# Kernel optimization log

Hardware: AMD Instinct MI355X
Metric: run time of the kernel (lower is better)

The kernel has to match this reference:

```python
import jax, jax.numpy as jnp
import numpy as np

B, T, C = 8, 2048, 1024  # batch, seq_len (== block_size), n_embed
HEAD = 64


def setup_inputs() -> dict:
    key = jax.random.key(0)
    k1, k2, k3, k4 = jax.random.split(key, 4)
    x = jax.random.normal(k1, (B, T, C), dtype=jnp.float32)
    # nn.Linear(n_embed, head_size, bias=False) -> weight [head, C]; stored as [C, head]
    Wk = jax.random.normal(k2, (C, HEAD), dtype=jnp.float32) * (C ** -0.5)
    Wq = jax.random.normal(k3, (C, HEAD), dtype=jnp.float32) * (C ** -0.5)
    Wv = jax.random.normal(k4, (C, HEAD), dtype=jnp.float32) * (C ** -0.5)
    return {"x": x, "Wk": Wk, "Wq": Wq, "Wv": Wv}


def reference(x, Wk, Wq, Wv):
    Bx, Tx, Cx = x.shape
    k = jnp.einsum('btc,ch->bth', x, Wk)  # [B,T,HEAD]
    q = jnp.einsum('btc,ch->bth', x, Wq)
    v = jnp.einsum('btc,ch->bth', x, Wv)
    # Source quirk: scores = k @ q^T (k rows), scaled by n_embed**-0.5 (C, not head_size)
    scores = jnp.einsum('bih,bjh->bij', k, q) * (Cx ** -0.5)  # [B,T,T]
    causal = jnp.tril(jnp.ones((Tx, Tx), dtype=bool))
    scores = jnp.where(causal, scores, -jnp.inf)
    attn = jax.nn.softmax(scores, axis=-1)
    out = jnp.einsum('bij,bjh->bih', attn, v)  # [B,T,HEAD]
    return out
```

## Files before the change

### kernel.cpp

```cpp
#include <hip/hip_runtime.h>
#include <cstdint>

#define B_ 8
#define T_ 2048
#define C_ 1024
#define H_ 64
#define BT_ (B_ * T_)

typedef short short8 __attribute__((ext_vector_type(8)));
typedef short bh4 __attribute__((ext_vector_type(4)));
typedef float f32x4 __attribute__((ext_vector_type(4)));

__device__ inline short f2bf(float f) {
  uint32_t u = __float_as_uint(f);
  u += 0x7fffu + ((u >> 16) & 1u);
  return (short)(u >> 16);
}

__device__ __forceinline__ void gl_lds16(const void* g, void* l) {
  __builtin_amdgcn_global_load_lds(
      (const __attribute__((address_space(1))) unsigned int*)g,
      (__attribute__((address_space(3))) unsigned int*)l, 16, 0, 0);
}

__global__ __launch_bounds__(256) void prep_w(
    const float* __restrict__ Wk, const float* __restrict__ Wq,
    const float* __restrict__ Wv, short* __restrict__ Wt) {
  __shared__ float wl[64][68];
  const int mat = blockIdx.x >> 4;
  const int kc = blockIdx.x & 15;
  const float* W = (mat == 0) ? Wk : (mat == 1) ? Wq : Wv;
  const float sc = (mat == 0) ? 0.03125f * 1.44269504088896f : 1.0f;
  const int t = threadIdx.x;
  const int k0 = kc * 64;
#pragma unroll
  for (int j = 0; j < 4; ++j) {
    int s = t + 256 * j;
    int kr = s >> 4, cf = s & 15;
    float4 v = *reinterpret_cast<const float4*>(&W[(size_t)(k0 + kr) * H_ + cf * 4]);
    wl[kr][cf * 4 + 0] = v.x; wl[kr][cf * 4 + 1] = v.y;
    wl[kr][cf * 4 + 2] = v.z; wl[kr][cf * 4 + 3] = v.w;
  }
  __syncthreads();
#pragma unroll
  for (int j = 0; j < 2; ++j) {
    int s = t + 256 * j;
    int n = s >> 3, g = s & 7;
    short8 o;
#pragma unroll
    for (int i = 0; i < 8; ++i) o[i] = f2bf(wl[8 * g + i][n] * sc);
    *reinterpret_cast<short8*>(&Wt[(size_t)(mat * 64 + n) * C_ + k0 + 8 * g]) = o;
  }
}

__global__ __launch_bounds__(256, 1) void proj_kernel(
    const float* __restrict__ x, const short* __restrict__ Wt,
    short* __restrict__ Kp, short* __restrict__ Qp, short* __restrict__ Vt) {
  __shared__ float xs[2][32 * 64];
  __shared__ short ws[2][192 * 64];
  const int t = threadIdx.x;
  const int w = t >> 6, lane = t & 63;
  const int l15 = lane & 15, lg = lane >> 4;
  const int rg = w >> 1, ch = w & 1;
  const int rowBase = blockIdx.x * 32;

  f32x4 acc[6];
  const f32x4 zf = {0.f, 0.f, 0.f, 0.f};
#pragma unroll
  for (int i = 0; i < 6; ++i) acc[i] = zf;

  auto stage = [&](int buf, int k0) {
#pragma unroll
    for (int j = 0; j < 2; ++j) {
      const int seg = w * 2 + j;
      const int r = seg * 4 + (lane >> 4);
      const float* g =
          &x[(size_t)(rowBase + r) * C_ + k0 + (((lane & 15) ^ (r & 7)) << 2)];
      gl_lds16(g, (char*)&xs[buf][0] + seg * 1024);
    }
#pragma unroll
    for (int j = 0; j < 6; ++j) {
      const int seg = w * 6 + j;
      const int n = seg * 8 + (lane >> 3);
      const short* g =
          &Wt[(size_t)n * C_ + k0 + (((lane & 7) ^ (n & 7)) << 3)];
      gl_lds16(g, (char*)&ws[buf][0] + seg * 1024);
    }
  };

  stage(0, 0);

#pragma unroll 1
  for (int it = 0; it < 16; ++it) {
    __syncthreads();
    const int cb = it & 1;
    if (it < 15) stage(cb ^ 1, (it + 1) * 64);
    const int arow = 16 * rg + l15;
    const int x7 = arow & 7;
    const float* xrow = &xs[cb][arow * 64];
    float4 fa = *reinterpret_cast<const float4*>(xrow + (((2 * lg) ^ x7) << 2));
    float4 fb = *reinterpret_cast<const float4*>(xrow + (((2 * lg + 1) ^ x7) << 2));
    float4 fc = *reinterpret_cast<const float4*>(xrow + (((2 * lg + 8) ^ x7) << 2));
    float4 fd = *reinterpret_cast<const float4*>(xrow + (((2 * lg + 9) ^ x7) << 2));
    short8 a0, a1;
    a0[0] = f2bf(fa.x); a0[1] = f2bf(fa.y); a0[2] = f2bf(fa.z); a0[3] = f2bf(fa.w);
    a0[4] = f2bf(fb.x); a0[5] = f2bf(fb.y); a0[6] = f2bf(fb.z); a0[7] = f2bf(fb.w);
    a1[0] = f2bf(fc.x); a1[1] = f2bf(fc.y); a1[2] = f2bf(fc.z); a1[3] = f2bf(fc.w);
    a1[4] = f2bf(fd.x); a1[5] = f2bf(fd.y); a1[6] = f2bf(fd.z); a1[7] = f2bf(fd.w);
#pragma unroll
    for (int nt = 0; nt < 6; ++nt) {
      const int n2 = 16 * (6 * ch + nt) + l15, n7 = n2 & 7;
      const short* wrow = &ws[cb][n2 * 64];
      short8 b0 = *reinterpret_cast<const short8*>(wrow + ((lg ^ n7) << 3));
      short8 b1 = *reinterpret_cast<const short8*>(wrow + (((4 + lg) ^ n7) << 3));
      acc[nt] = __builtin_amdgcn_mfma_f32_16x16x32_bf16(a0, b0, acc[nt], 0, 0, 0);
      acc[nt] = __builtin_amdgcn_mfma_f32_16x16x32_bf16(a1, b1, acc[nt], 0, 0, 0);
    }
  }

  const int strip = blockIdx.x * 2 + rg;
  const int rb = strip * 16;
#pragma unroll
  for (int nt = 0; nt < 6; ++nt) {
    const int ntg = 6 * ch + nt;
    if (ntg < 8) {
      short* O = (ntg < 4) ? Kp : Qp;
      const int col = (ntg & 3) * 16 + l15;
#pragma unroll
      for (int r = 0; r < 4; ++r)
        O[(size_t)(rb + lg * 4 + r) * H_ + col] = f2bf(acc[nt][r]);
    }
  }
  __syncthreads();
  if (ch == 1) {
    short* vl = reinterpret_cast<short*>(&xs[0][0]) + rg * (16 * 66);
#pragma unroll
    for (int nt = 2; nt < 6; ++nt)
#pragma unroll
      for (int r = 0; r < 4; ++r)
        vl[(lg * 4 + r) * 66 + (nt - 2) * 16 + l15] = f2bf(acc[nt][r]);
    asm volatile("s_waitcnt lgkmcnt(0)" ::: "memory");
    short8 o0, o1;
#pragma unroll
    for (int i = 0; i < 8; ++i) o0[i] = vl[i * 66 + lane];
#pragma unroll
    for (int i = 0; i < 8; ++i) o1[i] = vl[(8 + i) * 66 + lane];
    const int bb = strip >> 7, tb = (strip & 127) * 16;
    short* dst = &Vt[((size_t)bb * H_ + lane) * T_ + tb];
    *reinterpret_cast<short8*>(dst) = o0;
    *reinterpret_cast<short8*>(dst + 8) = o1;
  }
}

__global__ __launch_bounds__(512) void attn_kernel(
    const short* __restrict__ Kq, const short* __restrict__ Qk,
    const short* __restrict__ Vt, float* __restrict__ Pg,
    float* __restrict__ Mg) {
  __shared__ short Ks[4][64 * 64];
  __shared__ short Vs[4][64 * 64];
  const int t = threadIdx.x, w = t >> 6, lane = t & 63;
  const int l15 = lane & 15, lg = lane >> 4;
  const int batch = blockIdx.x & 7;
  const int rest = blockIdx.x >> 3;
  const int qh = rest & 3;
  const int g = rest >> 2;
  const int sidx = (g < 8) ? (15 - g) : (g - 8);
  const int rg = w;
  const short* Kb = Kq + (size_t)batch * T_ * H_;
  const short* Qb = Qk + (size_t)batch * T_ * H_;
  const short* Vb = Vt + (size_t)batch * H_ * T_;
  const f32x4 zf = {0.f, 0.f, 0.f, 0.f};
  const int k7 = l15 & 7;

  const int qbase = sidx * 128;
  const int qrow = qbase + rg * 16 + l15;
  const short8 qa0 = *reinterpret_cast<const short8*>(&Kb[(size_t)qrow * H_ + lg * 8]);
  const short8 qa1 = *reinterpret_cast<const short8*>(&Kb[(size_t)qrow * H_ + lg * 8 + 32]);
  const int ntop = 2 * sidx + 1;
  const int nlist = (ntop >= qh) ? (((ntop - qh) >> 2) + 1) : 0;
  const int np = (nlist + 1) >> 1;

  const int tp = w >> 2, kind = (w >> 1) & 1, q2 = w & 1;
  const int srow = lane >> 3;
  const int ssw = ((lane & 7) ^ srow) << 3;
  auto stage = [&](int per) {
    const int le = 2 * per + tp;
    if (le >= nlist) return;
    const int gkt = 4 * le + qh;
    const int buf = (per & 1) * 2 + tp;
    const int kbase = gkt * 64;
    if (kind == 0) {
#pragma unroll
      for (int g2 = 0; g2 < 4; ++g2) {
        const int gg = q2 * 4 + g2;
        gl_lds16(&Qb[(size_t)(kbase + gg * 8 + srow) * H_ + ssw],
                 (char*)&Ks[buf][0] + gg * 1024);
      }
    } else {
#pragma unroll
      for (int g2 = 0; g2 < 4; ++g2) {
        const int gg = q2 * 4 + g2;
        gl_lds16(&Vb[(size_t)(gg * 8 + srow) * T_ + kbase + ssw],
                 (char*)&Vs[buf][0] + gg * 1024);
      }
    }
  };

  f32x4 O[4];
#pragma unroll
  for (int i = 0; i < 4; ++i) O[i] = zf;
  float m = -1e30f, l = 0.f;

  stage(0);

#pragma unroll 1
  for (int i = 0; i < np; ++i) {
    __syncthreads();
    if (i + 1 < np) stage(i + 1);
#pragma unroll 1
    for (int tt = 0; tt < 2; ++tt) {
      const int le = 2 * i + tt;
      if (le < nlist) {
        const int gkt = 4 * le + qh;
        const int cb = (i & 1) * 2 + tt;
        const int kbase = gkt * 64;
        f32x4 S[4];
        __builtin_amdgcn_s_setprio(1);
#pragma unroll
        for (int nt = 0; nt < 4; ++nt) {
          S[nt] = zf;
          const short* krow = &Ks[cb][(16 * nt + l15) * 64];
          short8 kf0 = *reinterpret_cast<const short8*>(&krow[(lg ^ k7) << 3]);
          short8 kf1 = *reinterpret_cast<const short8*>(&krow[((4 + lg) ^ k7) << 3]);
          S[nt] = __builtin_amdgcn_mfma_f32_16x16x32_bf16(kf0, qa0, S[nt], 0, 0, 0);
          S[nt] = __builtin_amdgcn_mfma_f32_16x16x32_bf16(kf1, qa1, S[nt], 0, 0, 0);
        }
        __builtin_amdgcn_s_setprio(0);
        if (gkt >= 2 * sidx) {
#pragma unroll
          for (int nt = 0; nt < 4; ++nt) {
            const int klo = kbase + 16 * nt + 4 * lg;
#pragma unroll
            for (int r = 0; r < 4; ++r)
              if (klo + r > qrow) S[nt][r] = -1e30f;
          }
        }
        float mx0 = fmaxf(fmaxf(S[0][0], S[0][1]), fmaxf(S[0][2], S[0][3]));
        float mx1 = fmaxf(fmaxf(S[1][0], S[1][1]), fmaxf(S[1][2], S[1][3]));
        float mx2 = fmaxf(fmaxf(S[2][0], S[2][1]), fmaxf(S[2][2], S[2][3]));
        float mx3 = fmaxf(fmaxf(S[3][0], S[3][1]), fmaxf(S[3][2], S[3][3]));
        float mx = fmaxf(fmaxf(mx0, mx1), fmaxf(mx2, mx3));
        mx = fmaxf(mx, __shfl_xor(mx, 16));
        mx = fmaxf(mx, __shfl_xor(mx, 32));
        const float mn = fmaxf(m, mx);
        const float scv = exp2f(m - mn);
        m = mn;
        float rs = 0.f;
#pragma unroll
        for (int nt = 0; nt < 4; ++nt)
#pragma unroll
          for (int r = 0; r < 4; ++r) {
            const float pv = exp2f(S[nt][r] - mn);
            S[nt][r] = pv;
            rs += pv;
          }
        rs += __shfl_xor(rs, 16);
        rs += __shfl_xor(rs, 32);
        l = l * scv + rs;
#pragma unroll
        for (int nt = 0; nt < 4; ++nt) O[nt] *= scv;
        const int d7 = l15 & 7;
        const int vo = 4 * (lg & 1);
        __builtin_amdgcn_s_setprio(1);
#pragma unroll
        for (int kc = 0; kc < 2; ++kc) {
          short8 pa;
#pragma unroll
          for (int jj = 0; jj < 8; ++jj)
            pa[jj] = f2bf(S[2 * kc + (jj >> 2)][jj & 3]);
          const int slo = ((4 * kc + (lg >> 1)) ^ d7) << 3;
          const int shi = ((4 * kc + 2 + (lg >> 1)) ^ d7) << 3;
#pragma unroll
          for (int nt = 0; nt < 4; ++nt) {
            const short* vrow = &Vs[cb][(16 * nt + l15) * 64];
            const bh4 vlo = *reinterpret_cast<const bh4*>(&vrow[slo + vo]);
            const bh4 vhi = *reinterpret_cast<const bh4*>(&vrow[shi + vo]);
            short8 vf;
            vf[0] = vlo[0]; vf[1] = vlo[1]; vf[2] = vlo[2]; vf[3] = vlo[3];
            vf[4] = vhi[0]; vf[5] = vhi[1]; vf[6] = vhi[2]; vf[7] = vhi[3];
            O[nt] = __builtin_amdgcn_mfma_f32_16x16x32_bf16(vf, pa, O[nt], 0, 0, 0);
          }
        }
        __builtin_amdgcn_s_setprio(0);
      }
    }
  }

  const size_t gr = (size_t)batch * T_ + qrow;
#pragma unroll
  for (int nt = 0; nt < 4; ++nt)
    *reinterpret_cast<f32x4*>(&Pg[((size_t)qh * BT_ + gr) * H_ + 16 * nt + 4 * lg]) = O[nt];
  if (lg == 0) {
    Mg[((size_t)qh * BT_ + gr) * 2 + 0] = m;
    Mg[((size_t)qh * BT_ + gr) * 2 + 1] = l;
  }
}

__global__ __launch_bounds__(256) void combine_kernel(
    const float* __restrict__ Pg, const float* __restrict__ Mg,
    float* __restrict__ out) {
  const int t = threadIdx.x;
#pragma unroll
  for (int k = 0; k < 2; ++k) {
    const int task = blockIdx.x * 512 + k * 256 + t;
    const int row = task >> 4;
    const int c4 = task & 15;
    float Mh[4], Lh[4];
#pragma unroll
    for (int h = 0; h < 4; ++h) {
      Mh[h] = Mg[((size_t)h * BT_ + row) * 2 + 0];
      Lh[h] = Mg[((size_t)h * BT_ + row) * 2 + 1];
    }
    const float M = fmaxf(fmaxf(Mh[0], Mh[1]), fmaxf(Mh[2], Mh[3]));
    float L = 0.f;
    f32x4 o = {0.f, 0.f, 0.f, 0.f};
#pragma unroll
    for (int h = 0; h < 4; ++h) {
      const float e = exp2f(Mh[h] - M);
      L += Lh[h] * e;
      const f32x4 po =
          *reinterpret_cast<const f32x4*>(&Pg[((size_t)h * BT_ + row) * H_ + c4 * 4]);
      o += po * e;
    }
    const f32x4 res = o * (1.f / L);
    *reinterpret_cast<f32x4*>(&out[(size_t)row * H_ + c4 * 4]) = res;
  }
}

extern "C" void kernel_launch(void* const* d_in, const int* in_sizes, int n_in,
                              void* d_out, int out_size, void* d_ws, size_t ws_size,
                              hipStream_t stream) {
  const float* x = (const float*)d_in[0];
  const float* Wk = (const float*)d_in[1];
  const float* Wq = (const float*)d_in[2];
  const float* Wv = (const float*)d_in[3];
  float* out = (float*)d_out;

  short* Kp = (short*)d_ws;
  short* Qp = Kp + (size_t)BT_ * H_;
  short* Vt = Qp + (size_t)BT_ * H_;
  short* Wt = Vt + (size_t)BT_ * H_;
  float* Pg = (float*)(Wt + 192 * C_);
  float* Mg = Pg + (size_t)4 * BT_ * H_;

  hipLaunchKernelGGL(prep_w, dim3(48), dim3(256), 0, stream, Wk, Wq, Wv, Wt);
  hipLaunchKernelGGL(proj_kernel, dim3(512), dim3(256), 0, stream, x, Wt, Kp, Qp, Vt);
  hipLaunchKernelGGL(attn_kernel, dim3(512), dim3(512), 0, stream, Kp, Qp, Vt, Pg, Mg);
  hipLaunchKernelGGL(combine_kernel, dim3(512), dim3(256), 0, stream, Pg, Mg, out);
}
```

Before: 52.56 us.

## Pre-swizzle weights into MFMA fragment layout and load directly to registers

prep_w now writes the bf16 projection weights in a layout that matches the per-lane MFMA B-fragment order. proj_kernel drops the LDS staging of weights and loads each wave's 12 B-fragments straight from global memory into registers with inline-asm dwordx4 loads, using manual vmcnt waits. This removes LDS traffic, shared-memory footprint and LDS reads for weights. In exchange each wave re-reads weights from L2 every iteration without double buffering, so global load latency sits on the critical path.

```diff
diff --git a/kernel.cpp b/kernel.cpp
--- a/kernel.cpp
+++ b/kernel.cpp
@@ -23,9 +23,13 @@
       (__attribute__((address_space(3))) unsigned int*)l, 16, 0, 0);
 }
 
+#define ALOADO(dst, p, off)                                        \
+  asm volatile("global_load_dwordx4 %0, %1, off offset:" #off      \
+               : "=v"(dst) : "v"(p) : "memory")
+
 __global__ __launch_bounds__(256) void prep_w(
     const float* __restrict__ Wk, const float* __restrict__ Wq,
-    const float* __restrict__ Wv, short* __restrict__ Wt) {
+    const float* __restrict__ Wv, short* __restrict__ Wp) {
   __shared__ float wl[64][68];
   const int mat = blockIdx.x >> 4;
   const int kc = blockIdx.x & 15;
@@ -49,15 +53,19 @@
     short8 o;
 #pragma unroll
     for (int i = 0; i < 8; ++i) o[i] = f2bf(wl[8 * g + i][n] * sc);
-    *reinterpret_cast<short8*>(&Wt[(size_t)(mat * 64 + n) * C_ + k0 + 8 * g]) = o;
+    const int ng = mat * 64 + n;
+    const int nt = ng >> 4, l15c = ng & 15;
+    const int f = g >> 2, lg2 = g & 3;
+    short* dst = Wp + (((size_t)(kc * 12 + nt) * 2 + f) << 9) +
+                 ((lg2 << 4) + l15c) * 8;
+    *reinterpret_cast<short8*>(dst) = o;
   }
 }
 
 __global__ __launch_bounds__(256, 1) void proj_kernel(
-    const float* __restrict__ x, const short* __restrict__ Wt,
+    const float* __restrict__ x, const short* __restrict__ Wp,
     short* __restrict__ Kp, short* __restrict__ Qp, short* __restrict__ Vt) {
   __shared__ float xs[2][32 * 64];
-  __shared__ short ws[2][192 * 64];
   const int t = threadIdx.x;
   const int w = t >> 6, lane = t & 63;
   const int l15 = lane & 15, lg = lane >> 4;
@@ -69,7 +77,7 @@
 #pragma unroll
   for (int i = 0; i < 6; ++i) acc[i] = zf;
 
-  auto stage = [&](int buf, int k0) {
+  auto stageX = [&](int buf, int k0) {
 #pragma unroll
     for (int j = 0; j < 2; ++j) {
       const int seg = w * 2 + j;
@@ -78,23 +86,34 @@
           &x[(size_t)(rowBase + r) * C_ + k0 + (((lane & 15) ^ (r & 7)) << 2)];
       gl_lds16(g, (char*)&xs[buf][0] + seg * 1024);
     }
-#pragma unroll
-    for (int j = 0; j < 6; ++j) {
-      const int seg = w * 6 + j;
-      const int n = seg * 8 + (lane >> 3);
-      const short* g =
-          &Wt[(size_t)n * C_ + k0 + (((lane & 7) ^ (n & 7)) << 3)];
-      gl_lds16(g, (char*)&ws[buf][0] + seg * 1024);
-    }
   };
 
-  stage(0, 0);
+  stageX(0, 0);
 
 #pragma unroll 1
   for (int it = 0; it < 16; ++it) {
     __syncthreads();
     const int cb = it & 1;
-    if (it < 15) stage(cb ^ 1, (it + 1) * 64);
+    short8 bw[12];
+    const short* wb0 = Wp + (((size_t)(it * 12 + 6 * ch)) << 10) + lane * 8;
+    const short* wb1 = wb0 + 2048;
+    const short* wb2 = wb0 + 4096;
+    ALOADO(bw[0], wb0, 0);    ALOADO(bw[1], wb0, 1024);
+    ALOADO(bw[2], wb0, 2048); ALOADO(bw[3], wb0, 3072);
+    ALOADO(bw[4], wb1, 0);    ALOADO(bw[5], wb1, 1024);
+    ALOADO(bw[6], wb1, 2048); ALOADO(bw[7], wb1, 3072);
+    ALOADO(bw[8], wb2, 0);    ALOADO(bw[9], wb2, 1024);
+    ALOADO(bw[10], wb2, 2048); ALOADO(bw[11], wb2, 3072);
+    __builtin_amdgcn_sched_barrier(0);
+    if (it < 15) stageX(cb ^ 1, (it + 1) * 64);
+    __builtin_amdgcn_sched_barrier(0);
+    if (it < 15) {
+      asm volatile("s_waitcnt vmcnt(2)" ::: "memory");
+    } else {
+      asm volatile("s_waitcnt vmcnt(0)" ::: "memory");
+    }
+    __builtin_amdgcn_sched_barrier(0);
+
     const int arow = 16 * rg + l15;
     const int x7 = arow & 7;
     const float* xrow = &xs[cb][arow * 64];
@@ -109,12 +128,8 @@
     a1[4] = f2bf(fd.x); a1[5] = f2bf(fd.y); a1[6] = f2bf(fd.z); a1[7] = f2bf(fd.w);
 #pragma unroll
     for (int nt = 0; nt < 6; ++nt) {
-      const int n2 = 16 * (6 * ch + nt) + l15, n7 = n2 & 7;
-      const short* wrow = &ws[cb][n2 * 64];
-      short8 b0 = *reinterpret_cast<const short8*>(wrow + ((lg ^ n7) << 3));
-      short8 b1 = *reinterpret_cast<const short8*>(wrow + (((4 + lg) ^ n7) << 3));
-      acc[nt] = __builtin_amdgcn_mfma_f32_16x16x32_bf16(a0, b0, acc[nt], 0, 0, 0);
-      acc[nt] = __builtin_amdgcn_mfma_f32_16x16x32_bf16(a1, b1, acc[nt], 0, 0, 0);
+      acc[nt] = __builtin_amdgcn_mfma_f32_16x16x32_bf16(a0, bw[2 * nt], acc[nt], 0, 0, 0);
+      acc[nt] = __builtin_amdgcn_mfma_f32_16x16x32_bf16(a1, bw[2 * nt + 1], acc[nt], 0, 0, 0);
     }
   }
 
@@ -349,12 +364,12 @@
   short* Kp = (short*)d_ws;
   short* Qp = Kp + (size_t)BT_ * H_;
   short* Vt = Qp + (size_t)BT_ * H_;
-  short* Wt = Vt + (size_t)BT_ * H_;
-  float* Pg = (float*)(Wt + 192 * C_);
+  short* Wp = Vt + (size_t)BT_ * H_;
+  float* Pg = (float*)(Wp + 192 * C_);
   float* Mg = Pg + (size_t)4 * BT_ * H_;
 
-  hipLaunchKernelGGL(prep_w, dim3(48), dim3(256), 0, stream, Wk, Wq, Wv, Wt);
-  hipLaunchKernelGGL(proj_kernel, dim3(512), dim3(256), 0, stream, x, Wt, Kp, Qp, Vt);
+  hipLaunchKernelGGL(prep_w, dim3(48), dim3(256), 0, stream, Wk, Wq, Wv, Wp);
+  hipLaunchKernelGGL(proj_kernel, dim3(512), dim3(256), 0, stream, x, Wp, Kp, Qp, Vt);
   hipLaunchKernelGGL(attn_kernel, dim3(512), dim3(512), 0, stream, Kp, Qp, Vt, Pg, Mg);
   hipLaunchKernelGGL(combine_kernel, dim3(512), dim3(256), 0, stream, Pg, Mg, out);
 }
```

Result: faster. 50.33 us (-4.2%).
